# Optimization experiments

Hardware: AMD Instinct MI355X
Metric: run time of the kernel (lower is better)

## Reference

```python
import jax, jax.numpy as jnp
import numpy as np

KERNEL = 301  # sliding max window length (odd -> same-size output)
TOPK = 2


def setup_inputs() -> dict:
    key = jax.random.key(0)
    xcorr = jax.random.normal(key, (32, 3, 64, 8192), dtype=jnp.float32)
    return {"xcorr": xcorr, "nlag": 4096}


def reference(xcorr, nlag):
    # xcorr: [nb, nc, nx, nt]
    x = jnp.abs(xcorr)  # vabs=True
    pad = KERNEL // 2
    # sliding-window max over time axis (== F.max_pool2d((1,K), stride 1, pad K//2))
    smax = jax.lax.reduce_window(
        x,
        -jnp.inf,
        jax.lax.max,
        window_dimensions=(1, 1, 1, KERNEL),
        window_strides=(1, 1, 1, 1),
        padding=[(0, 0), (0, 0), (0, 0), (pad, pad)],
    )
    # keep only local maxima, zero elsewhere (x * (smax == x).float())
    scores = jnp.where(smax == x, x, jnp.zeros((), x.dtype))
    topk_score, topk_idx = jax.lax.top_k(scores, TOPK)  # [nb, nc, nx, TOPK]
    return topk_score, topk_idx
```

## Files before the change

### kernel.cpp

```cpp
#include <hip/hip_runtime.h>
#include <stdint.h>


#define NT 8192
#define RADIUS 150
#define NSEG 256
#define NTHREADS 256
#define CAND_CAP 1024

__global__ __launch_bounds__(256) void detect_peaks_kernel(
    const float* __restrict__ x, float* __restrict__ out, int nrows)
{
    const int row = blockIdx.x;
    const int tid = threadIdx.x;

    __shared__ __align__(16) float xs[NT];
    __shared__ float m[NSEG];
    __shared__ int cand[CAND_CAP];
    __shared__ int cnt;
    __shared__ unsigned long long wred[8];

    if (tid == 0) cnt = 0;

    const float4* g = (const float4*)(x + (size_t)row * NT);
    float4 vv[8];
#pragma unroll
    for (int it = 0; it < 8; ++it) {
        float4 v = g[it * 256 + tid];
        v.x = fabsf(v.x); v.y = fabsf(v.y); v.z = fabsf(v.z); v.w = fabsf(v.w);
        vv[it] = v;
        float cm = fmaxf(fmaxf(v.x, v.y), fmaxf(v.z, v.w));
        cm = fmaxf(cm, __shfl_xor(cm, 1));
        cm = fmaxf(cm, __shfl_xor(cm, 2));
        cm = fmaxf(cm, __shfl_xor(cm, 4));
        const int c = it * 256 + tid;
        ((float4*)xs)[c] = v;
        if ((tid & 7) == 0) m[c >> 3] = cm;
    }
    __syncthreads();

#pragma unroll
    for (int it = 0; it < 8; ++it) {
        const int c = it * 256 + tid;
        const float ms = m[c >> 3];
        const float4 v = vv[it];
        const int base = c * 4;
        if (v.x == ms) { int p = atomicAdd(&cnt, 1); if (p < CAND_CAP) cand[p] = base + 0; }
        if (v.y == ms) { int p = atomicAdd(&cnt, 1); if (p < CAND_CAP) cand[p] = base + 1; }
        if (v.z == ms) { int p = atomicAdd(&cnt, 1); if (p < CAND_CAP) cand[p] = base + 2; }
        if (v.w == ms) { int p = atomicAdd(&cnt, 1); if (p < CAND_CAP) cand[p] = base + 3; }
    }
    __syncthreads();

    const int ncand = min(cnt, CAND_CAP);
    unsigned long long k1 = 0ull, k2 = 0ull;

    for (int k = tid; k < ncand; k += NTHREADS) {
        const int t = cand[k];
        const float v = xs[t];
        const int l = max(t - RADIUS, 0);
        const int r = min(t + RADIUS, NT - 1);
        const int il = l >> 5, ir = r >> 5;
        float wmax = 0.0f;
        for (int s = il + 1; s < ir; ++s) wmax = fmaxf(wmax, m[s]);
        const int le = (il << 5) + 32;
        for (int u = l; u < le; ++u) wmax = fmaxf(wmax, xs[u]);
        const int rs = ir << 5;
        for (int u = rs; u <= r; ++u) wmax = fmaxf(wmax, xs[u]);
        if (v >= wmax) {
            const unsigned long long key =
                ((unsigned long long)__float_as_uint(v) << 32) |
                (unsigned)(NT - 1 - t);
            if (key > k1) { k2 = k1; k1 = key; }
            else if (key > k2) { k2 = key; }
        }
    }

#pragma unroll
    for (int off = 32; off >= 1; off >>= 1) {
        unsigned long long o1 = __shfl_down(k1, off);
        unsigned long long o2 = __shfl_down(k2, off);
        unsigned long long hi = (k1 > o1) ? k1 : o1;
        unsigned long long lo = (k1 > o1) ? o1 : k1;
        unsigned long long s2 = (k2 > o2) ? k2 : o2;
        k1 = hi;
        k2 = (lo > s2) ? lo : s2;
    }
    const int wave = tid >> 6;
    if ((tid & 63) == 0) { wred[wave * 2] = k1; wred[wave * 2 + 1] = k2; }
    __syncthreads();

    if (tid == 0) {
        unsigned long long a1 = wred[0], a2 = wred[1];
        for (int w = 1; w < 4; ++w) {
            unsigned long long o1 = wred[w * 2], o2 = wred[w * 2 + 1];
            unsigned long long hi = (a1 > o1) ? a1 : o1;
            unsigned long long lo = (a1 > o1) ? o1 : a1;
            unsigned long long s2 = (a2 > o2) ? a2 : o2;
            a1 = hi;
            a2 = (lo > s2) ? lo : s2;
        }
        float s1v, s2v; int i1, i2;
        if (a1 == 0ull) { s1v = 0.0f; i1 = 0; }
        else {
            s1v = __uint_as_float((unsigned)(a1 >> 32));
            i1 = (NT - 1) - (int)(a1 & 0xffffffffull);
        }
        if (a2 == 0ull) {
            s2v = 0.0f;
            i2 = (i1 == 0) ? 1 : 0;
        } else {
            s2v = __uint_as_float((unsigned)(a2 >> 32));
            i2 = (NT - 1) - (int)(a2 & 0xffffffffull);
        }
        out[row * 2 + 0] = s1v;
        out[row * 2 + 1] = s2v;
        float* oi = out + (size_t)nrows * 2;
        oi[row * 2 + 0] = (float)i1;
        oi[row * 2 + 1] = (float)i2;
    }
}

extern "C" void kernel_launch(void* const* d_in, const int* in_sizes, int n_in,
                              void* d_out, int out_size, void* d_ws, size_t ws_size,
                              hipStream_t stream) {
    const float* x = (const float*)d_in[0];
    float* out = (float*)d_out;
    const int nrows = in_sizes[0] / NT;
    detect_peaks_kernel<<<nrows, NTHREADS, 0, stream>>>(x, out, nrows);
}
```

Baseline: 306.7 us.

## Replace shared candidate list with in-register peak checks using 4-element maxima

Drops the 32KB shared copy of the row and the atomic candidate list, and keeps a shared array of per-float4 maxima plus per-32 segment maxima instead. Each thread checks its own chunk-local maxima directly: it scans segment maxima first for an early exit, then uses the 4-element maxima for the edges and reads the few unaligned edge elements back from global memory. This lowers shared memory use, which can raise occupancy, and removes the atomics and one barrier. The cost is that candidate work is spread unevenly across threads and the edge elements come from global memory.

```diff
diff --git a/kernel.cpp b/kernel.cpp
--- a/kernel.cpp
+++ b/kernel.cpp
@@ -4,9 +4,7 @@
 
 #define NT 8192
 #define RADIUS 150
-#define NSEG 256
 #define NTHREADS 256
-#define CAND_CAP 1024
 
 __global__ __launch_bounds__(256) void detect_peaks_kernel(
     const float* __restrict__ x, float* __restrict__ out, int nrows)
@@ -14,62 +12,68 @@
     const int row = blockIdx.x;
     const int tid = threadIdx.x;
 
-    __shared__ __align__(16) float xs[NT];
-    __shared__ float m[NSEG];
-    __shared__ int cand[CAND_CAP];
-    __shared__ int cnt;
+    __shared__ float m4[NT / 4];
+    __shared__ float m[NT / 32];
     __shared__ unsigned long long wred[8];
 
-    if (tid == 0) cnt = 0;
+    const float* grow = x + (size_t)row * NT;
+    const float4* g4 = (const float4*)grow;
 
-    const float4* g = (const float4*)(x + (size_t)row * NT);
     float4 vv[8];
 #pragma unroll
+    for (int it = 0; it < 8; ++it) vv[it] = g4[it * 256 + tid];
+
+    float cms[8];
+#pragma unroll
     for (int it = 0; it < 8; ++it) {
-        float4 v = g[it * 256 + tid];
+        float4 v = vv[it];
         v.x = fabsf(v.x); v.y = fabsf(v.y); v.z = fabsf(v.z); v.w = fabsf(v.w);
         vv[it] = v;
-        float cm = fmaxf(fmaxf(v.x, v.y), fmaxf(v.z, v.w));
-        cm = fmaxf(cm, __shfl_xor(cm, 1));
+        const int c = it * 256 + tid;
+        float cm4 = fmaxf(fmaxf(v.x, v.y), fmaxf(v.z, v.w));
+        m4[c] = cm4;
+        float cm = fmaxf(cm4, __shfl_xor(cm4, 1));
         cm = fmaxf(cm, __shfl_xor(cm, 2));
         cm = fmaxf(cm, __shfl_xor(cm, 4));
-        const int c = it * 256 + tid;
-        ((float4*)xs)[c] = v;
+        cms[it] = cm;
         if ((tid & 7) == 0) m[c >> 3] = cm;
     }
     __syncthreads();
 
+    unsigned long long k1 = 0ull, k2 = 0ull;
+
 #pragma unroll
     for (int it = 0; it < 8; ++it) {
-        const int c = it * 256 + tid;
-        const float ms = m[c >> 3];
+        const float cm = cms[it];
         const float4 v = vv[it];
-        const int base = c * 4;
-        if (v.x == ms) { int p = atomicAdd(&cnt, 1); if (p < CAND_CAP) cand[p] = base + 0; }
-        if (v.y == ms) { int p = atomicAdd(&cnt, 1); if (p < CAND_CAP) cand[p] = base + 1; }
-        if (v.z == ms) { int p = atomicAdd(&cnt, 1); if (p < CAND_CAP) cand[p] = base + 2; }
-        if (v.w == ms) { int p = atomicAdd(&cnt, 1); if (p < CAND_CAP) cand[p] = base + 3; }
-    }
-    __syncthreads();
-
-    const int ncand = min(cnt, CAND_CAP);
-    unsigned long long k1 = 0ull, k2 = 0ull;
-
-    for (int k = tid; k < ncand; k += NTHREADS) {
-        const int t = cand[k];
-        const float v = xs[t];
-        const int l = max(t - RADIUS, 0);
-        const int r = min(t + RADIUS, NT - 1);
-        const int il = l >> 5, ir = r >> 5;
-        float wmax = 0.0f;
-        for (int s = il + 1; s < ir; ++s) wmax = fmaxf(wmax, m[s]);
-        const int le = (il << 5) + 32;
-        for (int u = l; u < le; ++u) wmax = fmaxf(wmax, xs[u]);
-        const int rs = ir << 5;
-        for (int u = rs; u <= r; ++u) wmax = fmaxf(wmax, xs[u]);
-        if (v >= wmax) {
+        const int base = (it * 256 + tid) * 4;
+#pragma unroll
+        for (int e = 0; e < 4; ++e) {
+            const float val = (e == 0) ? v.x : (e == 1) ? v.y : (e == 2) ? v.z : v.w;
+            if (val != cm) continue;
+            const int t = base + e;
+            const int l = max(t - RADIUS, 0);
+            const int r = min(t + RADIUS, NT - 1);
+            const int il = l >> 5, ir = r >> 5;
+            float im = 0.0f;
+            for (int s = il + 1; s < ir; ++s) im = fmaxf(im, m[s]);
+            if (im > val) continue;
+            float em = 0.0f;
+            {
+                const int le4 = (il + 1) << 3;
+                const int fb = (l + 3) >> 2;
+                for (int u = l; u < fb * 4; ++u) em = fmaxf(em, fabsf(grow[u]));
+                for (int b = fb; b < le4; ++b) em = fmaxf(em, m4[b]);
+            }
+            {
+                const int rs4 = ir << 3;
+                const int re = (r + 1) & ~3;
+                for (int b = rs4; b < (re >> 2); ++b) em = fmaxf(em, m4[b]);
+                for (int u = re; u <= r; ++u) em = fmaxf(em, fabsf(grow[u]));
+            }
+            if (em > val) continue;
             const unsigned long long key =
-                ((unsigned long long)__float_as_uint(v) << 32) |
+                ((unsigned long long)__float_as_uint(val) << 32) |
                 (unsigned)(NT - 1 - t);
             if (key > k1) { k2 = k1; k1 = key; }
             else if (key > k2) { k2 = key; }
```

Result: slower. 409.5 us (+33.5%).
